# Performance work log

Hardware: AMD Instinct MI355X
Metric: run time of the kernel (lower is better)

## Reference

```python
import jax, jax.numpy as jnp
import numpy as np

DIM = 256
NH = 4
HD = DIM // NH
RR = 8
EPS_BN = 1e-5


def dwconv(x, w, b):
    # depthwise conv, stride 1, SAME padding (odd kernel, pad=k//2)
    out = jax.lax.conv_general_dilated(
        x, w, window_strides=(1, 1), padding='SAME',
        feature_group_count=x.shape[1],
        dimension_numbers=('NCHW', 'OIHW', 'NCHW'))
    return out + b[None, :, None, None]


def conv1x1(x, w, b):
    # w: [out_c, in_c]
    return jnp.einsum('bchw,oc->bohw', x, w) + b[None, :, None, None]


def bn_eval(x, g, be, m, v):
    inv = g / jnp.sqrt(v + EPS_BN)
    return x * inv[None, :, None, None] + (be - m * inv)[None, :, None, None]


def l2norm(x):
    n = jnp.sqrt(jnp.sum(x * x, axis=-1, keepdims=True))
    return x / jnp.maximum(n, 1e-12)


def setup_inputs() -> dict:
    key = jax.random.key(0)
    ks = jax.random.split(key, 32)
    d = {}
    d['x1'] = jax.random.normal(ks[0], (8, DIM, 64, 64), jnp.float32)
    d['x2'] = jax.random.normal(ks[1], (8, DIM, 64, 64), jnp.float32)
    # multi-scale depthwise convs k=3,5,7
    for i, k in enumerate([3, 5, 7]):
        d[f'ms_w{k}'] = jax.random.normal(ks[2 + i], (DIM, 1, k, k), jnp.float32) * (1.0 / k)
        d[f'ms_b{k}'] = jax.random.normal(ks[5 + i], (DIM,), jnp.float32) * 0.02
    # qkv 1x1 conv + BN params for each stream
    for s, off in [(1, 8), (2, 16)]:
        d[f'qkv{s}_w'] = jax.random.normal(ks[off], (3 * DIM, DIM), jnp.float32) * (DIM ** -0.5)
        d[f'qkv{s}_b'] = jnp.zeros((3 * DIM,), jnp.float32)
        d[f'bn{s}_g'] = 1.0 + 0.1 * jax.random.normal(ks[off + 1], (3 * DIM,), jnp.float32)
        d[f'bn{s}_b'] = 0.1 * jax.random.normal(ks[off + 2], (3 * DIM,), jnp.float32)
        d[f'bn{s}_m'] = 0.1 * jax.random.normal(ks[off + 3], (3 * DIM,), jnp.float32)
        d[f'bn{s}_v'] = jax.random.uniform(ks[off + 4], (3 * DIM,), jnp.float32, 0.5, 1.5)
    # SE channel attention (shared module)
    d['ca_w1'] = jax.random.normal(ks[24], (DIM // RR, DIM), jnp.float32) * (DIM ** -0.5)
    d['ca_b1'] = jnp.zeros((DIM // RR,), jnp.float32)
    d['ca_w2'] = jax.random.normal(ks[25], (DIM, DIM // RR), jnp.float32) * ((DIM // RR) ** -0.5)
    d['ca_b2'] = jnp.zeros((DIM,), jnp.float32)
    # output projections
    d['po1_w'] = jax.random.normal(ks[26], (DIM, DIM), jnp.float32) * (DIM ** -0.5)
    d['po1_b'] = jnp.zeros((DIM,), jnp.float32)
    d['po2_w'] = jax.random.normal(ks[27], (DIM, DIM), jnp.float32) * (DIM ** -0.5)
    d['po2_b'] = jnp.zeros((DIM,), jnp.float32)
    return d


def _scfa(x1, x2, ms_w3, ms_b3, ms_w5, ms_b5, ms_w7, ms_b7,
          qkv1_w, qkv1_b, bn1_g, bn1_b, bn1_m, bn1_v,
          qkv2_w, qkv2_b, bn2_g, bn2_b, bn2_m, bn2_v,
          ca_w1, ca_b1, ca_w2, ca_b2, po1_w, po1_b, po2_w, po2_b):
    b, c, h, w = x1.shape
    temp = HD ** -0.5

    def multi_scale(x):
        return (dwconv(x, ms_w3, ms_b3) + dwconv(x, ms_w5, ms_b5) + dwconv(x, ms_w7, ms_b7)) / 3.0

    x1f = multi_scale(x1)
    x2f = multi_scale(x2)

    qkv1 = jax.nn.gelu(bn_eval(conv1x1(x1f, qkv1_w, qkv1_b), bn1_g, bn1_b, bn1_m, bn1_v), approximate=False)
    qkv2 = jax.nn.gelu(bn_eval(conv1x1(x2f, qkv2_w, qkv2_b), bn2_g, bn2_b, bn2_m, bn2_v), approximate=False)

    def split_heads(t):
        q, k, v = jnp.split(t, 3, axis=1)
        f = lambda z: z.reshape(b, NH, HD, h * w)
        return f(q), f(k), f(v)

    x1_q, x1_k, x1_v = split_heads(qkv1)
    x2_q, x2_k, x2_v = split_heads(qkv2)

    q1, k2 = l2norm(x1_q), l2norm(x2_k)
    q2, k1 = l2norm(x2_q), l2norm(x1_k)

    attn1 = jax.nn.softmax(jnp.einsum('bhcn,bhdn->bhcd', q1, k2) * temp, axis=-1)
    attn2 = jax.nn.softmax(jnp.einsum('bhcn,bhdn->bhcd', q2, k1) * temp, axis=-1)

    x1_out = jnp.einsum('bhcd,bhdn->bhcn', attn1, x1_v).reshape(b, c, h, w)
    x2_out = jnp.einsum('bhcd,bhdn->bhcn', attn2, x2_v).reshape(b, c, h, w)

    def se_gate(x):
        p = x.mean(axis=(2, 3))  # [b, c]
        y = jax.nn.relu(jnp.einsum('bc,rc->br', p, ca_w1) + ca_b1)
        y = jax.nn.sigmoid(jnp.einsum('br,cr->bc', y, ca_w2) + ca_b2)
        return y[:, :, None, None]

    x1_out = x1_out * se_gate(x1_out)
    x2_out = x2_out * se_gate(x2_out)

    x1_out = conv1x1(x1_out, po1_w, po1_b) + x1
    x2_out = conv1x1(x2_out, po2_w, po2_b) + x2
    return x1_out, x2_out


def reference(x1, x2, ms_w3, ms_b3, ms_w5, ms_b5, ms_w7, ms_b7,
              qkv1_w, qkv1_b, bn1_g, bn1_b, bn1_m, bn1_v,
              qkv2_w, qkv2_b, bn2_g, bn2_b, bn2_m, bn2_v,
              ca_w1, ca_b1, ca_w2, ca_b2, po1_w, po1_b, po2_w, po2_b):
    return _scfa(x1, x2, ms_w3, ms_b3, ms_w5, ms_b5, ms_w7, ms_b7,
                 qkv1_w, qkv1_b, bn1_g, bn1_b, bn1_m, bn1_v,
                 qkv2_w, qkv2_b, bn2_g, bn2_b, bn2_m, bn2_v,
                 ca_w1, ca_b1, ca_w2, ca_b2, po1_w, po1_b, po2_w, po2_b)
```

## Files before the change

### kernel.cpp

```cpp
#include <hip/hip_runtime.h>
#include <hip/hip_bf16.h>


#define NPIX 4096

typedef __attribute__((ext_vector_type(8))) short bfrag;
typedef __attribute__((ext_vector_type(4))) float f4acc;

#define GLDS16(g, l) __builtin_amdgcn_global_load_lds( \
    (const __attribute__((address_space(1))) unsigned int*)(g), \
    (__attribute__((address_space(3))) unsigned int*)(l), 16, 0, 0)

__device__ __forceinline__ float bf2f(unsigned short h) {
  return __uint_as_float(((unsigned)h) << 16);
}
__device__ __forceinline__ unsigned short f2bf(float f) {
  unsigned u = __float_as_uint(f);
  unsigned r = (u + 0x7FFFu + ((u >> 16) & 1u)) >> 16;
  return (unsigned short)r;
}
__device__ __forceinline__ float gelu_f(float x) {
  float z = x * (1.5957691216f + 0.0713548163f * x * x);
  return x / (1.0f + __expf(-z));
}

__global__ __launch_bounds__(256) void prep_kernel(
    const float* __restrict__ w3, const float* __restrict__ b3,
    const float* __restrict__ w5, const float* __restrict__ b5,
    const float* __restrict__ w7, const float* __restrict__ b7,
    const float* __restrict__ qb1, const float* __restrict__ g1,
    const float* __restrict__ be1, const float* __restrict__ m1,
    const float* __restrict__ v1,
    const float* __restrict__ qb2, const float* __restrict__ g2,
    const float* __restrict__ be2, const float* __restrict__ m2,
    const float* __restrict__ v2,
    float* __restrict__ weff, float* __restrict__ beff,
    float* __restrict__ alpha, float* __restrict__ beta)
{
  const int c = threadIdx.x;
  for (int ky = 0; ky < 7; ++ky)
    for (int kx = 0; kx < 7; ++kx) {
      float w = w7[c * 49 + ky * 7 + kx];
      if (ky >= 1 && ky <= 5 && kx >= 1 && kx <= 5)
        w += w5[c * 25 + (ky - 1) * 5 + (kx - 1)];
      if (ky >= 2 && ky <= 4 && kx >= 2 && kx <= 4)
        w += w3[c * 9 + (ky - 2) * 3 + (kx - 2)];
      weff[c * 49 + ky * 7 + kx] = w * (1.0f / 3.0f);
    }
  beff[c] = (b3[c] + b5[c] + b7[c]) * (1.0f / 3.0f);
  for (int o = c; o < 768; o += 256) {
    float inv1 = g1[o] / sqrtf(v1[o] + 1e-5f);
    alpha[o] = inv1;
    beta[o]  = qb1[o] * inv1 + be1[o] - m1[o] * inv1;
    float inv2 = g2[o] / sqrtf(v2[o] + 1e-5f);
    alpha[768 + o] = inv2;
    beta[768 + o]  = qb2[o] * inv2 + be2[o] - m2[o] * inv2;
  }
}

__global__ __launch_bounds__(256) void convert_w(
    const float* __restrict__ s1, const float* __restrict__ s2,
    unsigned short* __restrict__ d1, unsigned short* __restrict__ d2)
{
  int idx = blockIdx.x * 256 + threadIdx.x;
  d1[idx] = f2bf(s1[idx]);
  d2[idx] = f2bf(s2[idx]);
}

__global__ __launch_bounds__(256) void ms_conv(
    const float* __restrict__ x1, const float* __restrict__ x2,
    const float* __restrict__ weff, const float* __restrict__ beff,
    unsigned short* __restrict__ xf0, unsigned short* __restrict__ xf1)
{
  __shared__ float tile[5888];
  const int bc2 = blockIdx.x;
  const int s = bc2 >> 11, bc = bc2 & 2047;
  const int c = bc & 255;
  const int tid = threadIdx.x;
  const float* src = (s ? x2 : x1) + (size_t)bc * NPIX;
  float wreg[49];
#pragma unroll
  for (int i = 0; i < 49; ++i) wreg[i] = weff[c * 49 + i];
  const float bias = beff[c];
  float4 vv[4];
#pragma unroll
  for (int k = 0; k < 4; ++k)
    vv[k] = *(const float4*)&src[(k * 256 + tid) * 4];
#pragma unroll
  for (int k = 0; k < 4; ++k) {
    const int idx = k * 256 + tid;
    const int row = (idx >> 4) + 3;
    const int col = 4 + (idx & 15) * 4;
    *(float4*)&tile[84 * row + ((row >> 3) & 1) * 8 + col] = vv[k];
  }
  const float4 zq = {0.0f, 0.0f, 0.0f, 0.0f};
  for (int idx = tid; idx < 306; idx += 256) {
    int row, col;
    if (idx < 114) {
      int r6 = idx / 19;
      col = (idx - r6 * 19) * 4;
      row = (r6 < 3) ? r6 : (r6 + 64);
    } else {
      int j = idx - 114;
      int r64 = j / 3, q = j - r64 * 3;
      row = 3 + r64;
      col = (q == 0) ? 0 : (64 + q * 4);
    }
    *(float4*)&tile[84 * row + ((row >> 3) & 1) * 8 + col] = zq;
  }
  __syncthreads();
  const int x0 = (tid & 15) * 4;
  const int y0 = (tid >> 4) * 4;
  float acc[4][4];
#pragma unroll
  for (int yo = 0; yo < 4; ++yo)
#pragma unroll
    for (int xo = 0; xo < 4; ++xo) acc[yo][xo] = bias;
#pragma unroll
  for (int r = 0; r < 10; ++r) {
    const int row = y0 + r;
    const int rb = 84 * row + ((row >> 3) & 1) * 8 + x0;
    float seg[12];
    *(float4*)&seg[0] = *(const float4*)&tile[rb];
    *(float4*)&seg[4] = *(const float4*)&tile[rb + 4];
    *(float4*)&seg[8] = *(const float4*)&tile[rb + 8];
    const int yolo = (r >= 6) ? (r - 6) : 0;
    const int yohi = (r < 3) ? r : 3;
#pragma unroll
    for (int yo = 0; yo < 4; ++yo) {
      if (yo < yolo || yo > yohi) continue;
      const int ky = r - yo;
#pragma unroll
      for (int kx = 0; kx < 7; ++kx) {
        const float w = wreg[ky * 7 + kx];
#pragma unroll
        for (int xo = 0; xo < 4; ++xo)
          acc[yo][xo] = fmaf(w, seg[1 + xo + kx], acc[yo][xo]);
      }
    }
  }
  unsigned short* dst = (s ? xf1 : xf0) + (size_t)bc * NPIX;
#pragma unroll
  for (int yo = 0; yo < 4; ++yo) {
    ushort4 u;
    u.x = f2bf(acc[yo][0]); u.y = f2bf(acc[yo][1]);
    u.z = f2bf(acc[yo][2]); u.w = f2bf(acc[yo][3]);
    *(ushort4*)&dst[(y0 + yo) * 64 + x0] = u;
  }
}

__global__ __launch_bounds__(256) void transpose_bf16(
    const unsigned short* __restrict__ s0, unsigned short* __restrict__ d0,
    const unsigned short* __restrict__ s1, unsigned short* __restrict__ d1,
    long sb, long db)
{
  __shared__ unsigned short T[64][72];
  const int n0 = blockIdx.x * 64, c0 = blockIdx.y * 64;
  const int z = blockIdx.z, st = z >> 3, b = z & 7;
  const unsigned short* src = st ? s1 : s0;
  unsigned short* dst = st ? d1 : d0;
  const int t = threadIdx.x;
  const int rhi = t >> 4, c4 = (t & 15) * 4;
#pragma unroll
  for (int rr = 0; rr < 4; ++rr) {
    int row = rr * 16 + rhi;
    ushort4 u = *(const ushort4*)&src[(size_t)b * sb + (size_t)(c0 + row) * NPIX + n0 + c4];
    T[row][c4 + 0] = u.x; T[row][c4 + 1] = u.y;
    T[row][c4 + 2] = u.z; T[row][c4 + 3] = u.w;
  }
  __syncthreads();
#pragma unroll
  for (int rr = 0; rr < 4; ++rr) {
    int nrow = rr * 16 + rhi;
    ushort4 u;
    u.x = T[c4 + 0][nrow]; u.y = T[c4 + 1][nrow];
    u.z = T[c4 + 2][nrow]; u.w = T[c4 + 3][nrow];
    *(ushort4*)&dst[(size_t)b * db + (size_t)(n0 + nrow) * 256 + c0 + c4] = u;
  }
}

__global__ __launch_bounds__(256) void qkv_gemm(
    const unsigned short* __restrict__ W1, const unsigned short* __restrict__ W2,
    const unsigned short* __restrict__ X0, const unsigned short* __restrict__ X1,
    const float* __restrict__ alpha, const float* __restrict__ beta,
    unsigned short* __restrict__ q1, unsigned short* __restrict__ q2,
    float* __restrict__ ns)
{
  __shared__ unsigned short As[2][128 * 64];
  __shared__ unsigned short Bs[2][128 * 64];
  const int n0 = blockIdx.x * 128, o0 = blockIdx.y * 128;
  const int z = blockIdx.z, s = z >> 3, b = z & 7;
  const unsigned short* Wb = s ? W2 : W1;
  const unsigned short* Xt = s ? X1 : X0;
  unsigned short* qkv = s ? q2 : q1;
  const float* al = alpha + s * 768;
  const float* be = beta + s * 768;
  float* normsq = ns + s * 4096;
  const int tid = threadIdx.x, w = tid >> 6, lane = tid & 63;
  const int wm = (w & 1) * 64;
  const int wn = (w >> 1) * 64;
  const int lrow8 = lane >> 3;
  const int lcolsw = ((lane & 7) ^ lrow8) * 8;
  const int fslot = lane & 7;
  f4acc acc[4][4] = {};
  auto stage = [&](int buf, int kc) {
#pragma unroll
    for (int j = 0; j < 4; ++j) {
      int i = w * 4 + j;
      GLDS16(Wb + (size_t)(o0 + i * 8 + lrow8) * 256 + kc + lcolsw, &As[buf][i * 512]);
      GLDS16(Xt + (size_t)b * 1048576 + (size_t)(n0 + i * 8 + lrow8) * 256 + kc + lcolsw,
             &Bs[buf][i * 512]);
    }
  };
  stage(0, 0);
#pragma unroll
  for (int t = 0; t < 4; ++t) {
    const int cur = t & 1;
    if (t < 3) stage(cur ^ 1, (t + 1) * 64);
    if (t < 3) asm volatile("s_waitcnt vmcnt(8)" ::: "memory");
    else       asm volatile("s_waitcnt vmcnt(0)" ::: "memory");
    __builtin_amdgcn_s_barrier();
#pragma unroll
    for (int ks = 0; ks < 2; ++ks) {
      const int slot = ((ks * 4 + (lane >> 4)) ^ fslot) * 8;
      bfrag a[4], bb[4];
#pragma unroll
      for (int mt = 0; mt < 4; ++mt)
        a[mt] = *(const bfrag*)&Bs[cur][(wm + mt * 16 + (lane & 15)) * 64 + slot];
#pragma unroll
      for (int nt = 0; nt < 4; ++nt)
        bb[nt] = *(const bfrag*)&As[cur][(wn + nt * 16 + (lane & 15)) * 64 + slot];
#pragma unroll
      for (int mt = 0; mt < 4; ++mt)
#pragma unroll
        for (int nt = 0; nt < 4; ++nt)
          acc[mt][nt] = __builtin_amdgcn_mfma_f32_16x16x32_bf16(a[mt], bb[nt], acc[mt][nt], 0, 0, 0);
    }
    __builtin_amdgcn_s_barrier();
  }
#pragma unroll
  for (int nt = 0; nt < 4; ++nt) {
    const int o = o0 + wn + nt * 16 + (lane & 15);
    const float alv = al[o], bev = be[o];
    unsigned short* orow = qkv + ((size_t)b * 768 + o) * NPIX;
    float sq = 0.0f;
#pragma unroll
    for (int mt = 0; mt < 4; ++mt) {
      const int n = n0 + wm + mt * 16 + (lane >> 4) * 4;
      float v0 = gelu_f(acc[mt][nt][0] * alv + bev);
      float v1 = gelu_f(acc[mt][nt][1] * alv + bev);
      float v2 = gelu_f(acc[mt][nt][2] * alv + bev);
      float v3 = gelu_f(acc[mt][nt][3] * alv + bev);
      ushort4 u;
      u.x = f2bf(v0); u.y = f2bf(v1); u.z = f2bf(v2); u.w = f2bf(v3);
      *(ushort4*)&orow[n] = u;
      sq += v0 * v0 + v1 * v1 + v2 * v2 + v3 * v3;
    }
    if (o0 + wn + nt * 16 < 512) {
      sq += __shfl_xor(sq, 16);
      sq += __shfl_xor(sq, 32);
      if (lane < 16) atomicAdd(&normsq[b * 512 + o], sq);
    }
  }
}

__global__ __launch_bounds__(256) void spart_kernel(
    const unsigned short* __restrict__ qkv1, const unsigned short* __restrict__ qkv2,
    float* __restrict__ Sp0, float* __restrict__ Sp1)
{
  __shared__ unsigned short Qs[2][64 * 128];
  __shared__ unsigned short Ks[2][64 * 128];
  const int ck = blockIdx.x, h = blockIdx.y;
  const int z = blockIdx.z, s = z >> 3, b = z & 7;
  const unsigned short* qs = s ? qkv2 : qkv1;
  const unsigned short* kp = (s ? qkv1 : qkv2) + 256 * NPIX;
  float* Sp = s ? Sp1 : Sp0;
  const int tid = threadIdx.x, w = tid >> 6, lane = tid & 63;
  const int lrow16 = lane >> 4;
  const size_t qbase = ((size_t)b * 768 + h * 64) * NPIX;
  f4acc acc[4] = {};
  auto stage = [&](int buf, int it) {
    const int noff = ck * 512 + it * 128;
#pragma unroll
    for (int j = 0; j < 4; ++j) {
      int i = w * 4 + j;
      int row = i * 4 + lrow16;
      int colsw = ((lane & 15) ^ (row & 15)) * 8;
      GLDS16(qs + qbase + (size_t)row * NPIX + noff + colsw, &Qs[buf][i * 512]);
      GLDS16(kp + qbase + (size_t)row * NPIX + noff + colsw, &Ks[buf][i * 512]);
    }
  };
  stage(0, 0);
#pragma unroll
  for (int it = 0; it < 4; ++it) {
    const int cur = it & 1;
    if (it < 3) stage(cur ^ 1, it + 1);
    if (it < 3) asm volatile("s_waitcnt vmcnt(8)" ::: "memory");
    else        asm volatile("s_waitcnt vmcnt(0)" ::: "memory");
    __builtin_amdgcn_s_barrier();
#pragma unroll
    for (int kk = 0; kk < 4; ++kk) {
      const int slot = ((kk * 4 + (lane >> 4)) ^ (lane & 15)) * 8;
      bfrag bq = *(const bfrag*)&Qs[cur][(w * 16 + (lane & 15)) * 128 + slot];
#pragma unroll
      for (int mt = 0; mt < 4; ++mt) {
        bfrag ak = *(const bfrag*)&Ks[cur][(mt * 16 + (lane & 15)) * 128 + slot];
        acc[mt] = __builtin_amdgcn_mfma_f32_16x16x32_bf16(ak, bq, acc[mt], 0, 0, 0);
      }
    }
    __builtin_amdgcn_s_barrier();
  }
  float* dst = Sp + ((size_t)(ck * 32) + b * 4 + h) * 4096;
  const int c = w * 16 + (lane & 15);
#pragma unroll
  for (int mt = 0; mt < 4; ++mt)
    *(float4*)&dst[c * 64 + mt * 16 + (lane >> 4) * 4] = *(float4*)&acc[mt];
}

__global__ __launch_bounds__(256) void softattn(
    const float* __restrict__ Sp0, const float* __restrict__ Sp1,
    const float* __restrict__ ns,
    unsigned short* __restrict__ at0, unsigned short* __restrict__ at1)
{
  const int bh2 = blockIdx.x;
  const int s = bh2 >> 5, bh = bh2 & 31;
  const int b = bh >> 2, h = bh & 3;
  const float* Sp = s ? Sp1 : Sp0;
  const float* nsq = ns + s * 4096;
  const float* nsk = ns + (s ^ 1) * 4096;
  unsigned short* attn = s ? at1 : at0;
  const int wv = threadIdx.x >> 6, lane = threadIdx.x & 63;
  const float ikd = 1.0f / fmaxf(sqrtf(nsk[b * 512 + 256 + h * 64 + lane]), 1e-12f);
  for (int c = wv; c < 64; c += 4) {
    float sm = 0.0f;
#pragma unroll
    for (int ch = 0; ch < 8; ++ch)
      sm += Sp[((size_t)(ch * 32) + bh) * 4096 + c * 64 + lane];
    const float iq = 1.0f / fmaxf(sqrtf(nsq[b * 512 + h * 64 + c]), 1e-12f);
    float zv = sm * 0.125f * iq * ikd;
    float m = zv;
#pragma unroll
    for (int off = 32; off > 0; off >>= 1) m = fmaxf(m, __shfl_xor(m, off));
    float e = expf(zv - m);
    float sum = e;
#pragma unroll
    for (int off = 32; off > 0; off >>= 1) sum += __shfl_xor(sum, off);
    attn[(size_t)bh * 4096 + c * 64 + lane] = f2bf(e / sum);
  }
}

__global__ __launch_bounds__(256) void av_kernel(
    const unsigned short* __restrict__ vt0, const unsigned short* __restrict__ vt1,
    const unsigned short* __restrict__ at0, const unsigned short* __restrict__ at1,
    unsigned short* __restrict__ xo0, unsigned short* __restrict__ xo1,
    long db, float* __restrict__ pool)
{
  __shared__ unsigned short Vs[256 * 64];
  __shared__ unsigned short At[64 * 64];
  const int n0 = blockIdx.x * 256, h = blockIdx.y;
  const int z = blockIdx.z, s = z >> 3, b = z & 7;
  const unsigned short* vt = s ? vt1 : vt0;
  const unsigned short* attn = s ? at1 : at0;
  unsigned short* xout = s ? xo1 : xo0;
  float* pl = pool + s * 2048;
  const int tid = threadIdx.x, w = tid >> 6, lane = tid & 63;
  const int lrow8 = lane >> 3;
  const int lcolsw = ((lane & 7) ^ lrow8) * 8;
  const int bh = b * 4 + h;
#pragma unroll
  for (int j = 0; j < 8; ++j) {
    int i = w * 8 + j;
    GLDS16(vt + ((size_t)b * 1048576 + (size_t)(n0 + i * 8 + lrow8) * 256) + h * 64 + lcolsw,
           &Vs[i * 512]);
  }
#pragma unroll
  for (int j = 0; j < 2; ++j) {
    int i = w * 2 + j;
    GLDS16(attn + (size_t)bh * 4096 + (size_t)(i * 8 + lrow8) * 64 + lcolsw, &At[i * 512]);
  }
  __syncthreads();
  f4acc acc[4][4] = {};
#pragma unroll
  for (int ks = 0; ks < 2; ++ks) {
    const int slot = ((ks * 4 + (lane >> 4)) ^ (lane & 7)) * 8;
    bfrag a[4], bb[4];
#pragma unroll
    for (int mt = 0; mt < 4; ++mt)
      a[mt] = *(const bfrag*)&At[(mt * 16 + (lane & 15)) * 64 + slot];
#pragma unroll
    for (int nt = 0; nt < 4; ++nt)
      bb[nt] = *(const bfrag*)&Vs[(w * 64 + nt * 16 + (lane & 15)) * 64 + slot];
#pragma unroll
    for (int mt = 0; mt < 4; ++mt)
#pragma unroll
      for (int nt = 0; nt < 4; ++nt)
        acc[mt][nt] = __builtin_amdgcn_mfma_f32_16x16x32_bf16(a[mt], bb[nt], acc[mt][nt], 0, 0, 0);
  }
#pragma unroll
  for (int mt = 0; mt < 4; ++mt) {
    const int c = mt * 16 + (lane >> 4) * 4;
    float s0 = 0.0f, s1 = 0.0f, s2 = 0.0f, s3 = 0.0f;
#pragma unroll
    for (int nt = 0; nt < 4; ++nt) {
      const int np = n0 + w * 64 + nt * 16 + (lane & 15);
      ushort4 u;
      u.x = f2bf(acc[mt][nt][0]); u.y = f2bf(acc[mt][nt][1]);
      u.z = f2bf(acc[mt][nt][2]); u.w = f2bf(acc[mt][nt][3]);
      *(ushort4*)&xout[(size_t)b * db + (size_t)np * 256 + h * 64 + c] = u;
      s0 += acc[mt][nt][0]; s1 += acc[mt][nt][1];
      s2 += acc[mt][nt][2]; s3 += acc[mt][nt][3];
    }
    s0 += __shfl_xor(s0, 1); s0 += __shfl_xor(s0, 2); s0 += __shfl_xor(s0, 4); s0 += __shfl_xor(s0, 8);
    s1 += __shfl_xor(s1, 1); s1 += __shfl_xor(s1, 2); s1 += __shfl_xor(s1, 4); s1 += __shfl_xor(s1, 8);
    s2 += __shfl_xor(s2, 1); s2 += __shfl_xor(s2, 2); s2 += __shfl_xor(s2, 4); s2 += __shfl_xor(s2, 8);
    s3 += __shfl_xor(s3, 1); s3 += __shfl_xor(s3, 2); s3 += __shfl_xor(s3, 4); s3 += __shfl_xor(s3, 8);
    if ((lane & 15) == 0) {
      atomicAdd(&pl[b * 256 + h * 64 + c + 0], s0);
      atomicAdd(&pl[b * 256 + h * 64 + c + 1], s1);
      atomicAdd(&pl[b * 256 + h * 64 + c + 2], s2);
      atomicAdd(&pl[b * 256 + h * 64 + c + 3], s3);
    }
  }
}

__global__ __launch_bounds__(256) void segate_scale(
    const float* __restrict__ pool, const float* __restrict__ w1,
    const float* __restrict__ b1, const float* __restrict__ w2,
    const float* __restrict__ b2,
    const float* __restrict__ W1, const float* __restrict__ W2,
    unsigned short* __restrict__ Wg)
{
  const int b16 = blockIdx.x;
  const int tid = threadIdx.x;
  __shared__ float p[256];
  __shared__ float hh[32];
  p[tid] = pool[b16 * 256 + tid] * (1.0f / 4096.0f);
  __syncthreads();
  if (tid < 32) {
    float s = b1[tid];
    for (int c = 0; c < 256; ++c) s = fmaf(w1[tid * 256 + c], p[c], s);
    hh[tid] = fmaxf(s, 0.0f);
  }
  __syncthreads();
  float s = b2[tid];
#pragma unroll
  for (int r = 0; r < 32; ++r) s = fmaf(w2[tid * 32 + r], hh[r], s);
  const float g = 1.0f / (1.0f + expf(-s));
  const float* W = (b16 >> 3) ? W2 : W1;
  for (int o = 0; o < 256; ++o)
    Wg[(size_t)b16 * 65536 + o * 256 + tid] = f2bf(W[o * 256 + tid] * g);
}

__global__ __launch_bounds__(256) void pout_gemm(
    const unsigned short* __restrict__ Wgall,
    const unsigned short* __restrict__ X0, const unsigned short* __restrict__ X1,
    long db, const float* __restrict__ bias0, const float* __restrict__ bias1,
    const float* __restrict__ xr0, const float* __restrict__ xr1,
    float* __restrict__ out)
{
  __shared__ unsigned short As[2][128 * 64];
  __shared__ unsigned short Bs[2][128 * 64];
  const int n0 = blockIdx.x * 128, o0 = blockIdx.y * 128;
  const int z = blockIdx.z, s = z >> 3, b = z & 7;
  const unsigned short* Wg = Wgall + (size_t)z * 65536;
  const unsigned short* Xt = s ? X1 : X0;
  const float* bias = s ? bias1 : bias0;
  const float* xresb = s ? xr1 : xr0;
  float* outb = out + (size_t)s * 8388608;
  const int tid = threadIdx.x, w = tid >> 6, lane = tid & 63;
  const int wm = (w & 1) * 64;
  const int wn = (w >> 1) * 64;
  const int lrow8 = lane >> 3;
  const int lcolsw = ((lane & 7) ^ lrow8) * 8;
  const int fslot = lane & 7;
  f4acc acc[4][4] = {};
  auto stage = [&](int buf, int kc) {
#pragma unroll
    for (int j = 0; j < 4; ++j) {
      int i = w * 4 + j;
      GLDS16(Wg + (size_t)(o0 + i * 8 + lrow8) * 256 + kc + lcolsw, &As[buf][i * 512]);
      GLDS16(Xt + (size_t)b * db + (size_t)(n0 + i * 8 + lrow8) * 256 + kc + lcolsw,
             &Bs[buf][i * 512]);
    }
  };
  stage(0, 0);
#pragma unroll
  for (int t = 0; t < 4; ++t) {
    const int cur = t & 1;
    if (t < 3) stage(cur ^ 1, (t + 1) * 64);
    if (t < 3) asm volatile("s_waitcnt vmcnt(8)" ::: "memory");
    else       asm volatile("s_waitcnt vmcnt(0)" ::: "memory");
    __builtin_amdgcn_s_barrier();
#pragma unroll
    for (int ks = 0; ks < 2; ++ks) {
      const int slot = ((ks * 4 + (lane >> 4)) ^ fslot) * 8;
      bfrag a[4], bb[4];
#pragma unroll
      for (int mt = 0; mt < 4; ++mt)
        a[mt] = *(const bfrag*)&Bs[cur][(wm + mt * 16 + (lane & 15)) * 64 + slot];
#pragma unroll
      for (int nt = 0; nt < 4; ++nt)
        bb[nt] = *(const bfrag*)&As[cur][(wn + nt * 16 + (lane & 15)) * 64 + slot];
#pragma unroll
      for (int mt = 0; mt < 4; ++mt)
#pragma unroll
        for (int nt = 0; nt < 4; ++nt)
          acc[mt][nt] = __builtin_amdgcn_mfma_f32_16x16x32_bf16(a[mt], bb[nt], acc[mt][nt], 0, 0, 0);
    }
    __builtin_amdgcn_s_barrier();
  }
#pragma unroll
  for (int nt = 0; nt < 4; ++nt) {
    const int o = o0 + wn + nt * 16 + (lane & 15);
    const float bi = bias[o];
    const float* res = xresb + ((size_t)b * 256 + o) * NPIX;
    float* orow = outb + ((size_t)b * 256 + o) * NPIX;
#pragma unroll
    for (int mt = 0; mt < 4; ++mt) {
      const int n = n0 + wm + mt * 16 + (lane >> 4) * 4;
      float4 r4 = *(const float4*)&res[n];
      float4 ov;
      ov.x = acc[mt][nt][0] + bi + r4.x;
      ov.y = acc[mt][nt][1] + bi + r4.y;
      ov.z = acc[mt][nt][2] + bi + r4.z;
      ov.w = acc[mt][nt][3] + bi + r4.w;
      *(float4*)&orow[n] = ov;
    }
  }
}

extern "C" void kernel_launch(void* const* d_in, const int* in_sizes, int n_in,
                              void* d_out, int out_size, void* d_ws, size_t ws_size,
                              hipStream_t stream) {
  const float* x1    = (const float*)d_in[0];
  const float* x2    = (const float*)d_in[1];
  const float* ms_w3 = (const float*)d_in[2];
  const float* ms_b3 = (const float*)d_in[3];
  const float* ms_w5 = (const float*)d_in[4];
  const float* ms_b5 = (const float*)d_in[5];
  const float* ms_w7 = (const float*)d_in[6];
  const float* ms_b7 = (const float*)d_in[7];
  const float* qkv1_w = (const float*)d_in[8];
  const float* qkv1_b = (const float*)d_in[9];
  const float* bn1_g = (const float*)d_in[10];
  const float* bn1_b = (const float*)d_in[11];
  const float* bn1_m = (const float*)d_in[12];
  const float* bn1_v = (const float*)d_in[13];
  const float* qkv2_w = (const float*)d_in[14];
  const float* qkv2_b = (const float*)d_in[15];
  const float* bn2_g = (const float*)d_in[16];
  const float* bn2_b = (const float*)d_in[17];
  const float* bn2_m = (const float*)d_in[18];
  const float* bn2_v = (const float*)d_in[19];
  const float* ca_w1 = (const float*)d_in[20];
  const float* ca_b1 = (const float*)d_in[21];
  const float* ca_w2 = (const float*)d_in[22];
  const float* ca_b2 = (const float*)d_in[23];
  const float* po1_w = (const float*)d_in[24];
  const float* po1_b = (const float*)d_in[25];
  const float* po2_w = (const float*)d_in[26];
  const float* po2_b = (const float*)d_in[27];

  char* ws = (char*)d_ws;
  float* weff  = (float*)(ws + 0);
  float* beff  = (float*)(ws + 51200);
  float* alpha = (float*)(ws + 53248);
  float* beta  = (float*)(ws + 59392);
  float* normsq = (float*)(ws + 65536);
  float* pool  = (float*)(ws + 98304);
  unsigned short* W1b = (unsigned short*)(ws + 131072);
  unsigned short* W2b = (unsigned short*)(ws + 524288);
  unsigned short* Wg  = (unsigned short*)(ws + 917504);
  unsigned short* attn1 = (unsigned short*)(ws + 3014656);
  unsigned short* attn2 = (unsigned short*)(ws + 3276800);
  float* Sp    = (float*)(ws + 3538944);
  unsigned short* xf   = (unsigned short*)(ws + 7733248);
  unsigned short* xf_t = (unsigned short*)(ws + 24510464);
  unsigned short* qkv1 = (unsigned short*)(ws + 41287680);
  unsigned short* qkv2 = (unsigned short*)(ws + 91619328);
  unsigned short* xf2   = (unsigned short*)d_out;
  unsigned short* xf2_t = (unsigned short*)((char*)d_out + 16777216);
  float* Sp2 = (float*)(ws + 7733248);
  unsigned short* v1t   = xf;
  unsigned short* v2t   = xf_t;
  unsigned short* xout1 = qkv2;
  unsigned short* xout2 = qkv1;
  const long QKV_BSTR = 768L * 4096;

  float* outf = (float*)d_out;

  prep_kernel<<<1, 256, 0, stream>>>(ms_w3, ms_b3, ms_w5, ms_b5, ms_w7, ms_b7,
                                     qkv1_b, bn1_g, bn1_b, bn1_m, bn1_v,
                                     qkv2_b, bn2_g, bn2_b, bn2_m, bn2_v,
                                     weff, beff, alpha, beta);
  convert_w<<<768, 256, 0, stream>>>(qkv1_w, qkv2_w, W1b, W2b);
  hipMemsetAsync(ws + 65536, 0, 49152, stream);

  ms_conv<<<4096, 256, 0, stream>>>(x1, x2, weff, beff, xf, xf2);
  transpose_bf16<<<dim3(64, 4, 16), 256, 0, stream>>>(xf, xf_t, xf2, xf2_t,
                                                      1048576L, 1048576L);
  qkv_gemm<<<dim3(32, 6, 16), 256, 0, stream>>>(W1b, W2b, xf_t, xf2_t,
                                                alpha, beta, qkv1, qkv2, normsq);

  spart_kernel<<<dim3(8, 4, 16), 256, 0, stream>>>(qkv1, qkv2, Sp, Sp2);
  softattn<<<64, 256, 0, stream>>>(Sp, Sp2, normsq, attn1, attn2);

  transpose_bf16<<<dim3(64, 4, 16), 256, 0, stream>>>(qkv1 + 512 * NPIX, v1t,
                                                      qkv2 + 512 * NPIX, v2t,
                                                      3145728L, 1048576L);

  av_kernel<<<dim3(16, 4, 16), 256, 0, stream>>>(v1t, v2t, attn1, attn2,
                                                 xout1, xout2, QKV_BSTR, pool);

  segate_scale<<<16, 256, 0, stream>>>(pool, ca_w1, ca_b1, ca_w2, ca_b2,
                                       po1_w, po2_w, Wg);

  pout_gemm<<<dim3(32, 2, 16), 256, 0, stream>>>(Wg, xout1, xout2, QKV_BSTR,
                                                 po1_b, po2_b, x1, x2, outf);
}
```

Baseline: 385.7 us.

## Load MFMA fragments directly from global memory, dropping LDS staging in GEMM kernels

Removes the LDS double-buffered global_load_lds staging and barriers from qkv_gemm, spart_kernel, av_kernel and pout_gemm. Each wave now reads its bf16 MFMA operand fragments straight from global memory and relies on L1/L2 for reuse across waves. Occupancy hints are added through launch_bounds min-blocks. This removes barrier and LDS traffic overhead and raises occupancy. The cost is redundant global/L2 reads, since each operand is now fetched by several waves, and less latency hiding from explicit prefetch.

```diff
diff --git a/kernel.cpp b/kernel.cpp
--- a/kernel.cpp
+++ b/kernel.cpp
@@ -6,10 +6,6 @@
 
 typedef __attribute__((ext_vector_type(8))) short bfrag;
 typedef __attribute__((ext_vector_type(4))) float f4acc;
-
-#define GLDS16(g, l) __builtin_amdgcn_global_load_lds( \
-    (const __attribute__((address_space(1))) unsigned int*)(g), \
-    (__attribute__((address_space(3))) unsigned int*)(l), 16, 0, 0)
 
 __device__ __forceinline__ float bf2f(unsigned short h) {
   return __uint_as_float(((unsigned)h) << 16);
@@ -179,19 +175,17 @@
   }
 }
 
-__global__ __launch_bounds__(256) void qkv_gemm(
+__global__ __launch_bounds__(256, 3) void qkv_gemm(
     const unsigned short* __restrict__ W1, const unsigned short* __restrict__ W2,
     const unsigned short* __restrict__ X0, const unsigned short* __restrict__ X1,
     const float* __restrict__ alpha, const float* __restrict__ beta,
     unsigned short* __restrict__ q1, unsigned short* __restrict__ q2,
     float* __restrict__ ns)
 {
-  __shared__ unsigned short As[2][128 * 64];
-  __shared__ unsigned short Bs[2][128 * 64];
   const int n0 = blockIdx.x * 128, o0 = blockIdx.y * 128;
   const int z = blockIdx.z, s = z >> 3, b = z & 7;
   const unsigned short* Wb = s ? W2 : W1;
-  const unsigned short* Xt = s ? X1 : X0;
+  const unsigned short* Xt = (s ? X1 : X0) + (size_t)b * 1048576;
   unsigned short* qkv = s ? q2 : q1;
   const float* al = alpha + s * 768;
   const float* be = beta + s * 768;
@@ -199,44 +193,26 @@
   const int tid = threadIdx.x, w = tid >> 6, lane = tid & 63;
   const int wm = (w & 1) * 64;
   const int wn = (w >> 1) * 64;
-  const int lrow8 = lane >> 3;
-  const int lcolsw = ((lane & 7) ^ lrow8) * 8;
-  const int fslot = lane & 7;
+  const int arow = lane & 15;
+  const int kg = (lane >> 4) * 8;
+  const unsigned short* Xb = Xt + (size_t)(n0 + wm + arow) * 256 + kg;
+  const unsigned short* Wp = Wb + (size_t)(o0 + wn + arow) * 256 + kg;
   f4acc acc[4][4] = {};
-  auto stage = [&](int buf, int kc) {
-#pragma unroll
-    for (int j = 0; j < 4; ++j) {
-      int i = w * 4 + j;
-      GLDS16(Wb + (size_t)(o0 + i * 8 + lrow8) * 256 + kc + lcolsw, &As[buf][i * 512]);
-      GLDS16(Xt + (size_t)b * 1048576 + (size_t)(n0 + i * 8 + lrow8) * 256 + kc + lcolsw,
-             &Bs[buf][i * 512]);
-    }
-  };
-  stage(0, 0);
-#pragma unroll
-  for (int t = 0; t < 4; ++t) {
-    const int cur = t & 1;
-    if (t < 3) stage(cur ^ 1, (t + 1) * 64);
-    if (t < 3) asm volatile("s_waitcnt vmcnt(8)" ::: "memory");
-    else       asm volatile("s_waitcnt vmcnt(0)" ::: "memory");
-    __builtin_amdgcn_s_barrier();
-#pragma unroll
-    for (int ks = 0; ks < 2; ++ks) {
-      const int slot = ((ks * 4 + (lane >> 4)) ^ fslot) * 8;
-      bfrag a[4], bb[4];
-#pragma unroll
-      for (int mt = 0; mt < 4; ++mt)
-        a[mt] = *(const bfrag*)&Bs[cur][(wm + mt * 16 + (lane & 15)) * 64 + slot];
+#pragma unroll 2
+  for (int kw = 0; kw < 8; ++kw) {
+    const int ko = kw * 32;
+    bfrag a[4], bb[4];
+#pragma unroll
+    for (int mt = 0; mt < 4; ++mt)
+      a[mt] = *(const bfrag*)&Xb[(size_t)(mt * 16) * 256 + ko];
+#pragma unroll
+    for (int nt = 0; nt < 4; ++nt)
+      bb[nt] = *(const bfrag*)&Wp[(size_t)(nt * 16) * 256 + ko];
+#pragma unroll
+    for (int mt = 0; mt < 4; ++mt)
 #pragma unroll
       for (int nt = 0; nt < 4; ++nt)
-        bb[nt] = *(const bfrag*)&As[cur][(wn + nt * 16 + (lane & 15)) * 64 + slot];
-#pragma unroll
-      for (int mt = 0; mt < 4; ++mt)
-#pragma unroll
-        for (int nt = 0; nt < 4; ++nt)
-          acc[mt][nt] = __builtin_amdgcn_mfma_f32_16x16x32_bf16(a[mt], bb[nt], acc[mt][nt], 0, 0, 0);
-    }
-    __builtin_amdgcn_s_barrier();
+        acc[mt][nt] = __builtin_amdgcn_mfma_f32_16x16x32_bf16(a[mt], bb[nt], acc[mt][nt], 0, 0, 0);
   }
 #pragma unroll
   for (int nt = 0; nt < 4; ++nt) {
@@ -264,51 +240,31 @@
   }
 }
 
-__global__ __launch_bounds__(256) void spart_kernel(
+__global__ __launch_bounds__(256, 4) void spart_kernel(
     const unsigned short* __restrict__ qkv1, const unsigned short* __restrict__ qkv2,
     float* __restrict__ Sp0, float* __restrict__ Sp1)
 {
-  __shared__ unsigned short Qs[2][64 * 128];
-  __shared__ unsigned short Ks[2][64 * 128];
   const int ck = blockIdx.x, h = blockIdx.y;
   const int z = blockIdx.z, s = z >> 3, b = z & 7;
   const unsigned short* qs = s ? qkv2 : qkv1;
   const unsigned short* kp = (s ? qkv1 : qkv2) + 256 * NPIX;
   float* Sp = s ? Sp1 : Sp0;
   const int tid = threadIdx.x, w = tid >> 6, lane = tid & 63;
-  const int lrow16 = lane >> 4;
+  const int arow = lane & 15;
+  const int kg = (lane >> 4) * 8;
   const size_t qbase = ((size_t)b * 768 + h * 64) * NPIX;
+  const unsigned short* Qb = qs + qbase + (size_t)(w * 16 + arow) * NPIX + ck * 512 + kg;
+  const unsigned short* Kb = kp + qbase + (size_t)arow * NPIX + ck * 512 + kg;
   f4acc acc[4] = {};
-  auto stage = [&](int buf, int it) {
-    const int noff = ck * 512 + it * 128;
-#pragma unroll
-    for (int j = 0; j < 4; ++j) {
-      int i = w * 4 + j;
-      int row = i * 4 + lrow16;
-      int colsw = ((lane & 15) ^ (row & 15)) * 8;
-      GLDS16(qs + qbase + (size_t)row * NPIX + noff + colsw, &Qs[buf][i * 512]);
-      GLDS16(kp + qbase + (size_t)row * NPIX + noff + colsw, &Ks[buf][i * 512]);
-    }
-  };
-  stage(0, 0);
-#pragma unroll
-  for (int it = 0; it < 4; ++it) {
-    const int cur = it & 1;
-    if (it < 3) stage(cur ^ 1, it + 1);
-    if (it < 3) asm volatile("s_waitcnt vmcnt(8)" ::: "memory");
-    else        asm volatile("s_waitcnt vmcnt(0)" ::: "memory");
-    __builtin_amdgcn_s_barrier();
-#pragma unroll
-    for (int kk = 0; kk < 4; ++kk) {
-      const int slot = ((kk * 4 + (lane >> 4)) ^ (lane & 15)) * 8;
-      bfrag bq = *(const bfrag*)&Qs[cur][(w * 16 + (lane & 15)) * 128 + slot];
-#pragma unroll
-      for (int mt = 0; mt < 4; ++mt) {
-        bfrag ak = *(const bfrag*)&Ks[cur][(mt * 16 + (lane & 15)) * 128 + slot];
-        acc[mt] = __builtin_amdgcn_mfma_f32_16x16x32_bf16(ak, bq, acc[mt], 0, 0, 0);
-      }
-    }
-    __builtin_amdgcn_s_barrier();
+#pragma unroll 4
+  for (int nw = 0; nw < 16; ++nw) {
+    const int no = nw * 32;
+    bfrag bq = *(const bfrag*)&Qb[no];
+#pragma unroll
+    for (int mt = 0; mt < 4; ++mt) {
+      bfrag ak = *(const bfrag*)&Kb[(size_t)(mt * 16) * NPIX + no];
+      acc[mt] = __builtin_amdgcn_mfma_f32_16x16x32_bf16(ak, bq, acc[mt], 0, 0, 0);
+    }
   }
   float* dst = Sp + ((size_t)(ck * 32) + b * 4 + h) * 4096;
   const int c = w * 16 + (lane & 15);
@@ -349,14 +305,12 @@
   }
 }
 
-__global__ __launch_bounds__(256) void av_kernel(
+__global__ __launch_bounds__(256, 3) void av_kernel(
     const unsigned short* __restrict__ vt0, const unsigned short* __restrict__ vt1,
     const unsigned short* __restrict__ at0, const unsigned short* __restrict__ at1,
     unsigned short* __restrict__ xo0, unsigned short* __restrict__ xo1,
     long db, float* __restrict__ pool)
 {
-  __shared__ unsigned short Vs[256 * 64];
-  __shared__ unsigned short At[64 * 64];
   const int n0 = blockIdx.x * 256, h = blockIdx.y;
   const int z = blockIdx.z, s = z >> 3, b = z & 7;
   const unsigned short* vt = s ? vt1 : vt0;
@@ -364,32 +318,23 @@
   unsigned short* xout = s ? xo1 : xo0;
   float* pl = pool + s * 2048;
   const int tid = threadIdx.x, w = tid >> 6, lane = tid & 63;
-  const int lrow8 = lane >> 3;
-  const int lcolsw = ((lane & 7) ^ lrow8) * 8;
+  const int arow = lane & 15;
+  const int kg = (lane >> 4) * 8;
   const int bh = b * 4 + h;
-#pragma unroll
-  for (int j = 0; j < 8; ++j) {
-    int i = w * 8 + j;
-    GLDS16(vt + ((size_t)b * 1048576 + (size_t)(n0 + i * 8 + lrow8) * 256) + h * 64 + lcolsw,
-           &Vs[i * 512]);
-  }
-#pragma unroll
-  for (int j = 0; j < 2; ++j) {
-    int i = w * 2 + j;
-    GLDS16(attn + (size_t)bh * 4096 + (size_t)(i * 8 + lrow8) * 64 + lcolsw, &At[i * 512]);
-  }
-  __syncthreads();
+  const unsigned short* Ab = attn + (size_t)bh * 4096 + (size_t)arow * 64 + kg;
+  const unsigned short* Vb = vt + (size_t)b * 1048576 +
+                             (size_t)(n0 + w * 64 + arow) * 256 + h * 64 + kg;
   f4acc acc[4][4] = {};
 #pragma unroll
   for (int ks = 0; ks < 2; ++ks) {
-    const int slot = ((ks * 4 + (lane >> 4)) ^ (lane & 7)) * 8;
+    const int ko = ks * 32;
     bfrag a[4], bb[4];
 #pragma unroll
     for (int mt = 0; mt < 4; ++mt)
-      a[mt] = *(const bfrag*)&At[(mt * 16 + (lane & 15)) * 64 + slot];
+      a[mt] = *(const bfrag*)&Ab[(size_t)(mt * 16) * 64 + ko];
 #pragma unroll
     for (int nt = 0; nt < 4; ++nt)
-      bb[nt] = *(const bfrag*)&Vs[(w * 64 + nt * 16 + (lane & 15)) * 64 + slot];
+      bb[nt] = *(const bfrag*)&Vb[(size_t)(nt * 16) * 256 + ko];
 #pragma unroll
     for (int mt = 0; mt < 4; ++mt)
 #pragma unroll
@@ -451,63 +396,43 @@
     Wg[(size_t)b16 * 65536 + o * 256 + tid] = f2bf(W[o * 256 + tid] * g);
 }
 
-__global__ __launch_bounds__(256) void pout_gemm(
+__global__ __launch_bounds__(256, 3) void pout_gemm(
     const unsigned short* __restrict__ Wgall,
     const unsigned short* __restrict__ X0, const unsigned short* __restrict__ X1,
     long db, const float* __restrict__ bias0, const float* __restrict__ bias1,
     const float* __restrict__ xr0, const float* __restrict__ xr1,
     float* __restrict__ out)
 {
-  __shared__ unsigned short As[2][128 * 64];
-  __shared__ unsigned short Bs[2][128 * 64];
   const int n0 = blockIdx.x * 128, o0 = blockIdx.y * 128;
   const int z = blockIdx.z, s = z >> 3, b = z & 7;
   const unsigned short* Wg = Wgall + (size_t)z * 65536;
-  const unsigned short* Xt = s ? X1 : X0;
+  const unsigned short* Xt = (s ? X1 : X0) + (size_t)b * db;
   const float* bias = s ? bias1 : bias0;
   const float* xresb = s ? xr1 : xr0;
   float* outb = out + (size_t)s * 8388608;
   const int tid = threadIdx.x, w = tid >> 6, lane = tid & 63;
   const int wm = (w & 1) * 64;
   const int wn = (w >> 1) * 64;
-  const int lrow8 = lane >> 3;
-  const int lcolsw = ((lane & 7) ^ lrow8) * 8;
-  const int fslot = lane & 7;
+  const int arow = lane & 15;
+  const int kg = (lane >> 4) * 8;
+  const unsigned short* Xb = Xt + (size_t)(n0 + wm + arow) * 256 + kg;
+  const unsigned short* Wp = Wg + (size_t)(o0 + wn + arow) * 256 + kg;
   f4acc acc[4][4] = {};
-  auto stage = [&](int buf, int kc) {
-#pragma unroll
-    for (int j = 0; j < 4; ++j) {
-      int i = w * 4 + j;
-      GLDS16(Wg + (size_t)(o0 + i * 8 + lrow8) * 256 + kc + lcolsw, &As[buf][i * 512]);
-      GLDS16(Xt + (size_t)b * db + (size_t)(n0 + i * 8 + lrow8) * 256 + kc + lcolsw,
-             &Bs[buf][i * 512]);
-    }
-  };
-  stage(0, 0);
-#pragma unroll
-  for (int t = 0; t < 4; ++t) {
-    const int cur = t & 1;
-    if (t < 3) stage(cur ^ 1, (t + 1) * 64);
-    if (t < 3) asm volatile("s_waitcnt vmcnt(8)" ::: "memory");
-    else       asm volatile("s_waitcnt vmcnt(0)" ::: "memory");
-    __builtin_amdgcn_s_barrier();
-#pragma unroll
-    for (int ks = 0; ks < 2; ++ks) {
-      const int slot = ((ks * 4 + (lane >> 4)) ^ fslot) * 8;
-      bfrag a[4], bb[4];
-#pragma unroll
-      for (int mt = 0; mt < 4; ++mt)
-        a[mt] = *(const bfrag*)&Bs[cur][(wm + mt * 16 + (lane & 15)) * 64 + slot];
+#pragma unroll 2
+  for (int kw = 0; kw < 8; ++kw) {
+    const int ko = kw * 32;
+    bfrag a[4], bb[4];
+#pragma unroll
+    for (int mt = 0; mt < 4; ++mt)
+      a[mt] = *(const bfrag*)&Xb[(size_t)(mt * 16) * 256 + ko];
+#pragma unroll
+    for (int nt = 0; nt < 4; ++nt)
+      bb[nt] = *(const bfrag*)&Wp[(size_t)(nt * 16) * 256 + ko];
+#pragma unroll
+    for (int mt = 0; mt < 4; ++mt)
 #pragma unroll
       for (int nt = 0; nt < 4; ++nt)
-        bb[nt] = *(const bfrag*)&As[cur][(wn + nt * 16 + (lane & 15)) * 64 + slot];
-#pragma unroll
-      for (int mt = 0; mt < 4; ++mt)
-#pragma unroll
-        for (int nt = 0; nt < 4; ++nt)
-          acc[mt][nt] = __builtin_amdgcn_mfma_f32_16x16x32_bf16(a[mt], bb[nt], acc[mt][nt], 0, 0, 0);
-    }
-    __builtin_amdgcn_s_barrier();
+        acc[mt][nt] = __builtin_amdgcn_mfma_f32_16x16x32_bf16(a[mt], bb[nt], acc[mt][nt], 0, 0, 0);
   }
 #pragma unroll
   for (int nt = 0; nt < 4; ++nt) {
```

Measured after the change: 463.5 us. +20.2%, slower.

## Enlarge qkv GEMM pixel tile to 256 and drop LDS double buffering

Applied to the files above, without the earlier changes.

The qkv GEMM block tile grows from 128x128 to 256 pixels by 128 outputs. Each wave now holds an 8x4 accumulator array, which reuses each weight fragment across more MFMAs and halves the number of blocks. The double-buffered LDS pipeline becomes a single buffer with full syncthreads around each stage, so global loads no longer overlap compute inside a block. Occupancy also drops from the extra registers and the 48KB of LDS per block.

```diff
diff --git a/kernel.cpp b/kernel.cpp
--- a/kernel.cpp
+++ b/kernel.cpp
@@ -186,9 +186,9 @@
     unsigned short* __restrict__ q1, unsigned short* __restrict__ q2,
     float* __restrict__ ns)
 {
-  __shared__ unsigned short As[2][128 * 64];
-  __shared__ unsigned short Bs[2][128 * 64];
-  const int n0 = blockIdx.x * 128, o0 = blockIdx.y * 128;
+  __shared__ unsigned short As[128 * 64];
+  __shared__ unsigned short Bs[256 * 64];
+  const int n0 = blockIdx.x * 256, o0 = blockIdx.y * 128;
   const int z = blockIdx.z, s = z >> 3, b = z & 7;
   const unsigned short* Wb = s ? W2 : W1;
   const unsigned short* Xt = s ? X1 : X0;
@@ -197,46 +197,49 @@
   const float* be = beta + s * 768;
   float* normsq = ns + s * 4096;
   const int tid = threadIdx.x, w = tid >> 6, lane = tid & 63;
-  const int wm = (w & 1) * 64;
+  const int wm = (w & 1) * 128;
   const int wn = (w >> 1) * 64;
   const int lrow8 = lane >> 3;
   const int lcolsw = ((lane & 7) ^ lrow8) * 8;
   const int fslot = lane & 7;
-  f4acc acc[4][4] = {};
-  auto stage = [&](int buf, int kc) {
+  f4acc acc[8][4] = {};
+  auto stage = [&](int kc) {
 #pragma unroll
     for (int j = 0; j < 4; ++j) {
       int i = w * 4 + j;
-      GLDS16(Wb + (size_t)(o0 + i * 8 + lrow8) * 256 + kc + lcolsw, &As[buf][i * 512]);
+      GLDS16(Wb + (size_t)(o0 + i * 8 + lrow8) * 256 + kc + lcolsw, &As[i * 512]);
+    }
+#pragma unroll
+    for (int j = 0; j < 8; ++j) {
+      int i = w * 8 + j;
       GLDS16(Xt + (size_t)b * 1048576 + (size_t)(n0 + i * 8 + lrow8) * 256 + kc + lcolsw,
-             &Bs[buf][i * 512]);
+             &Bs[i * 512]);
     }
   };
-  stage(0, 0);
+  stage(0);
 #pragma unroll
   for (int t = 0; t < 4; ++t) {
-    const int cur = t & 1;
-    if (t < 3) stage(cur ^ 1, (t + 1) * 64);
-    if (t < 3) asm volatile("s_waitcnt vmcnt(8)" ::: "memory");
-    else       asm volatile("s_waitcnt vmcnt(0)" ::: "memory");
-    __builtin_amdgcn_s_barrier();
+    __syncthreads();
 #pragma unroll
     for (int ks = 0; ks < 2; ++ks) {
       const int slot = ((ks * 4 + (lane >> 4)) ^ fslot) * 8;
-      bfrag a[4], bb[4];
-#pragma unroll
-      for (int mt = 0; mt < 4; ++mt)
-        a[mt] = *(const bfrag*)&Bs[cur][(wm + mt * 16 + (lane & 15)) * 64 + slot];
+      bfrag a[8], bb[4];
+#pragma unroll
+      for (int mt = 0; mt < 8; ++mt)
+        a[mt] = *(const bfrag*)&Bs[(wm + mt * 16 + (lane & 15)) * 64 + slot];
 #pragma unroll
       for (int nt = 0; nt < 4; ++nt)
-        bb[nt] = *(const bfrag*)&As[cur][(wn + nt * 16 + (lane & 15)) * 64 + slot];
-#pragma unroll
-      for (int mt = 0; mt < 4; ++mt)
+        bb[nt] = *(const bfrag*)&As[(wn + nt * 16 + (lane & 15)) * 64 + slot];
+#pragma unroll
+      for (int mt = 0; mt < 8; ++mt)
 #pragma unroll
         for (int nt = 0; nt < 4; ++nt)
           acc[mt][nt] = __builtin_amdgcn_mfma_f32_16x16x32_bf16(a[mt], bb[nt], acc[mt][nt], 0, 0, 0);
     }
-    __builtin_amdgcn_s_barrier();
+    if (t < 3) {
+      __syncthreads();
+      stage((t + 1) * 64);
+    }
   }
 #pragma unroll
   for (int nt = 0; nt < 4; ++nt) {
@@ -245,7 +248,7 @@
     unsigned short* orow = qkv + ((size_t)b * 768 + o) * NPIX;
     float sq = 0.0f;
 #pragma unroll
-    for (int mt = 0; mt < 4; ++mt) {
+    for (int mt = 0; mt < 8; ++mt) {
       const int n = n0 + wm + mt * 16 + (lane >> 4) * 4;
       float v0 = gelu_f(acc[mt][nt][0] * alv + bev);
       float v1 = gelu_f(acc[mt][nt][1] * alv + bev);
@@ -599,7 +602,7 @@
   ms_conv<<<4096, 256, 0, stream>>>(x1, x2, weff, beff, xf, xf2);
   transpose_bf16<<<dim3(64, 4, 16), 256, 0, stream>>>(xf, xf_t, xf2, xf2_t,
                                                       1048576L, 1048576L);
-  qkv_gemm<<<dim3(32, 6, 16), 256, 0, stream>>>(W1b, W2b, xf_t, xf2_t,
+  qkv_gemm<<<dim3(16, 6, 16), 256, 0, stream>>>(W1b, W2b, xf_t, xf2_t,
                                                 alpha, beta, qkv1, qkv2, normsq);
 
   spart_kernel<<<dim3(8, 4, 16), 256, 0, stream>>>(qkv1, qkv2, Sp, Sp2);
```

Result: slower. 401.3 us (+4.1%).
